# Performance work log

Hardware: AMD Instinct MI355X
Metric: run time of the kernel (lower is better)

The kernel has to match this reference:

```python
import jax, jax.numpy as jnp
import numpy as np

B = 4096          # batch
L = 4096          # lattice_size (64x64)
N = L // 2        # n_masked
H = 2048          # hidden_size


def setup_inputs() -> dict:
    key = jax.random.key(0)
    ks = jax.random.split(key, 4)
    scale = 0.02  # small init so exp(s) stays tame (s is already bounded by 2*tanh)
    x = jax.random.normal(ks[0], (B, L), dtype=jnp.float32)
    W1 = jax.random.normal(ks[1], (N, H), dtype=jnp.float32) * scale
    b1 = jnp.zeros((H,), jnp.float32)
    W2 = jax.random.normal(ks[2], (H, H), dtype=jnp.float32) * scale
    b2 = jnp.zeros((H,), jnp.float32)
    W3 = jax.random.normal(ks[3], (H, 2 * N), dtype=jnp.float32) * scale
    b3 = jnp.zeros((2 * N,), jnp.float32)
    # checkerboard mask: even sites frozen (masked), odd sites transformed
    idx_masked = jnp.arange(0, L, 2, dtype=jnp.int32)
    idx_unmasked = jnp.arange(1, L, 2, dtype=jnp.int32)
    return {"x": x, "W1": W1, "b1": b1, "W2": W2, "b2": b2,
            "W3": W3, "b3": b3,
            "idx_masked": idx_masked, "idx_unmasked": idx_unmasked}


def reference(x, W1, b1, W2, b2, W3, b3, idx_masked, idx_unmasked):
    # gather frozen half: (B, N)
    x_m = x[:, idx_masked]
    # 3-layer MLP with LeakyReLU(0.2)
    h = jax.nn.leaky_relu(x_m @ W1 + b1, negative_slope=0.2)
    h = jax.nn.leaky_relu(h @ W2 + b2, negative_slope=0.2)
    out = h @ W3 + b3                      # (B, 2N)
    s, t = out[:, :N], out[:, N:]
    s = 2.0 * jnp.tanh(s)
    # affine transform of the unmasked half, scatter back
    x_u = x[:, idx_unmasked]
    y_u = x_u * jnp.exp(s) + t
    y = x.at[:, idx_unmasked].set(y_u)
    log_det = s.sum(axis=1)                # (B,)
    return y, log_det
```

## Files before the change

kernel.cpp:

```cpp
#include <hip/hip_runtime.h>
#include <hip/hip_bf16.h>
#include <stdint.h>

#define MROWS 4096
#define LFULL 4096
#define NHALF 2048
#define HDIM  2048

typedef __bf16 bf16x8 __attribute__((ext_vector_type(8)));
typedef float  f32x4  __attribute__((ext_vector_type(4)));
typedef unsigned short u16x8 __attribute__((ext_vector_type(8)));

template<int V> struct ICt { static constexpr int value = V; };

__device__ __forceinline__ unsigned short f2bf(float f) {
    __hip_bfloat16 h = __float2bfloat16(f);
    return __builtin_bit_cast(unsigned short, h);
}
__device__ __forceinline__ float bf2f(unsigned short u) {
    return __builtin_bit_cast(float, (uint32_t)u << 16);
}
__device__ __forceinline__ float fast_tanh(float x) {
    float ax = fabsf(x);
    float e  = __expf(-2.0f * ax);
    float t  = (1.0f - e) / (1.0f + e);
    return copysignf(t, x);
}

__device__ __forceinline__ void gload_lds16(const void* g, void* l) {
    __builtin_amdgcn_global_load_lds(
        (const __attribute__((address_space(1))) uint32_t*)g,
        (__attribute__((address_space(3))) uint32_t*)l,
        16, 0, 0);
}

__global__ __launch_bounds__(256)
void cast_x_kernel(const float* __restrict__ x, __hip_bfloat16* __restrict__ xm,
                   float* __restrict__ ld)
{
    if (threadIdx.x == 0) ld[blockIdx.x] = 0.0f;
    size_t t = (size_t)blockIdx.x * 256 + threadIdx.x;
    size_t r = t >> 8;
    int    c = (int)(t & 255);
    const float4* xp = (const float4*)(x + r * LFULL + (size_t)c * 16);
    float4 a = xp[0], b = xp[1], d = xp[2], e = xp[3];
    u16x8 v;
    v[0] = f2bf(a.x); v[1] = f2bf(a.z);
    v[2] = f2bf(b.x); v[3] = f2bf(b.z);
    v[4] = f2bf(d.x); v[5] = f2bf(d.z);
    v[6] = f2bf(e.x); v[7] = f2bf(e.z);
    *(u16x8*)(xm + r * NHALF + (size_t)c * 8) = v;
}

template<bool PERM>
__global__ __launch_bounds__(256)
void transpose_cast_kernel(const float* __restrict__ W, __hip_bfloat16* __restrict__ WT,
                           int K, int N)
{
    __shared__ unsigned short lds[64][66];
    const int t  = threadIdx.x;
    const int k0 = blockIdx.y * 64;
    const int n0 = blockIdx.x * 64;

    #pragma unroll
    for (int it = 0; it < 4; ++it) {
        int kl = it * 16 + (t >> 4);
        int nl = (t & 15) * 4;
        float4 v = *(const float4*)(W + (size_t)(k0 + kl) * N + n0 + nl);
        lds[kl][nl + 0] = f2bf(v.x);
        lds[kl][nl + 1] = f2bf(v.y);
        lds[kl][nl + 2] = f2bf(v.z);
        lds[kl][nl + 3] = f2bf(v.w);
    }
    __syncthreads();

    int nl = t >> 2;
    int kc = (t & 3) * 16;
    unsigned short tmp[16];
    #pragma unroll
    for (int j = 0; j < 16; ++j) tmp[j] = lds[kc + j][nl];
    int jc = n0 + nl;
    int dstrow;
    if (PERM) {
        int half = jc >> 11;
        int j    = jc & 2047;
        int g = j >> 7, w = j & 127;
        int q = w >> 5, rest = w & 31, f = rest >> 4, c = rest & 15;
        dstrow = g * 256 + q * 64 + (f + 2 * half) * 16 + c;
    } else {
        dstrow = jc;
    }
    u16x8* dst = (u16x8*)(WT + (size_t)dstrow * K + k0 + kc);
    dst[0] = *(u16x8*)&tmp[0];
    dst[1] = *(u16x8*)&tmp[8];
}

template<int BM, int BN, int KD, int NOUT, bool RELU, bool FUSED>
__global__ __launch_bounds__(512, 2)
void gemm8p(const __hip_bfloat16* __restrict__ A,
            const __hip_bfloat16* __restrict__ BT,
            const float* __restrict__ bias,
            __hip_bfloat16* __restrict__ C,
            const float* __restrict__ xg,
            float* __restrict__ yg,
            float* __restrict__ ldg)
{
    constexpr int MF = BM / 32, NF = BN / 64, MH = MF / 2, NH = NF / 2;
    constexpr int LA = BM / 128, LB = BN / 128;
    constexpr int NT = KD / 64;
    constexpr int ABYTES = BM * 128, BBYTES = BN * 128;
    constexpr int BBASE = 2 * ABYTES;
    __shared__ __align__(1024) char lds[2 * ABYTES + 2 * BBYTES];

    const int tid  = threadIdx.x;
    const int wave = tid >> 6, lane = tid & 63;
    const int wm = wave >> 2, wn = wave & 3;
    const int l15 = lane & 15, lhi = lane >> 4;

    const int nwg = gridDim.x;
    const int bid = blockIdx.x;
    const int wg  = (bid & 7) * (nwg >> 3) + (bid >> 3);
    constexpr int NBN = NOUT / BN;
    const int bm = wg / NBN, bn = wg % NBN;

    const __hip_bfloat16* gA = A  + (size_t)(bm * BM) * KD;
    const __hip_bfloat16* gB = BT + (size_t)(bn * BN) * KD;

    const int srow = tid >> 3;
    const int scol = ((tid & 7) ^ (srow & 7)) * 8;
    char* sd = lds + srow * 128 + (tid & 7) * 16;

    const __hip_bfloat16* pA = gA + (size_t)srow * KD + scol;
    const __hip_bfloat16* pB = gB + (size_t)srow * KD + scol;

    #pragma unroll
    for (int s = 0; s < LB; ++s) gload_lds16(pB + (size_t)(s * 64) * KD,             sd + BBASE + s * 8192);
    #pragma unroll
    for (int s = 0; s < LB; ++s) gload_lds16(pB + (size_t)(BN/2 + s * 64) * KD,      sd + BBASE + (BN/2) * 128 + s * 8192);
    #pragma unroll
    for (int s = 0; s < LA; ++s) gload_lds16(pA + (size_t)(s * 64) * KD,             sd + s * 8192);
    #pragma unroll
    for (int s = 0; s < LA; ++s) gload_lds16(pA + (size_t)(BM/2 + s * 64) * KD,      sd + (BM/2) * 128 + s * 8192);
    #pragma unroll
    for (int s = 0; s < LB; ++s) gload_lds16(pB + 64 + (size_t)(s * 64) * KD,        sd + BBASE + BBYTES + s * 8192);
    #pragma unroll
    for (int s = 0; s < LB; ++s) gload_lds16(pB + 64 + (size_t)(BN/2 + s * 64) * KD, sd + BBASE + BBYTES + (BN/2) * 128 + s * 8192);
    pA += 64; pB += 128;
    asm volatile("s_waitcnt vmcnt(4)" ::: "memory");
    __builtin_amdgcn_s_barrier();

    const int arow0 = wm * (BM / 2) + l15;
    const int brow0 = wn * (BN / 4) + l15;
    const int swz   = (l15 & 7) << 4;
    const int colX[2] = { (lhi * 16) ^ swz, (64 + lhi * 16) ^ swz };
    const char* rA = lds + arow0 * 128;
    const char* rB = lds + brow0 * 128;

    bf16x8 af[MH][2], bf0[NH][2], bf1[NH][2];
    f32x4 acc[MF][NF] = {};

    #pragma unroll
    for (int m = 0; m < MH; ++m)
        #pragma unroll
        for (int kk = 0; kk < 2; ++kk)
            af[m][kk] = *(const bf16x8*)(rA + colX[kk] + m * 2048);
    #pragma unroll
    for (int n = 0; n < NH; ++n)
        #pragma unroll
        for (int kk = 0; kk < 2; ++kk)
            bf0[n][kk] = *(const bf16x8*)(rB + colX[kk] + (BBASE + n * 2048));

    auto body = [&](int t, auto bufc) {
        constexpr int BUF   = decltype(bufc)::value;
        constexpr int ABUF  = BUF * ABYTES;
        constexpr int ABUFo = (BUF ^ 1) * ABYTES;
        constexpr int BBUF  = BBASE + BUF * BBYTES;
        constexpr int BBUFo = BBASE + (BUF ^ 1) * BBYTES;

        if (t + 1 < NT) {
            #pragma unroll
            for (int s = 0; s < LA; ++s)
                gload_lds16(pA + (size_t)(s * 64) * KD, sd + ABUFo + s * 8192);
        }
        __builtin_amdgcn_s_setprio(1);
        #pragma unroll
        for (int kk = 0; kk < 2; ++kk)
            #pragma unroll
            for (int m = 0; m < MH; ++m)
                #pragma unroll
                for (int n = 0; n < NH; ++n)
                    acc[m][n] = __builtin_amdgcn_mfma_f32_16x16x32_bf16(af[m][kk], bf0[n][kk], acc[m][n], 0, 0, 0);
        __builtin_amdgcn_s_setprio(0);
        #pragma unroll
        for (int n = 0; n < NH; ++n)
            #pragma unroll
            for (int kk = 0; kk < 2; ++kk)
                bf1[n][kk] = *(const bf16x8*)(rB + colX[kk] + (BBUF + (NH + n) * 2048));
        __builtin_amdgcn_s_barrier();

        if (t + 1 < NT) {
            #pragma unroll
            for (int s = 0; s < LA; ++s)
                gload_lds16(pA + (size_t)(BM/2 + s * 64) * KD, sd + ABUFo + (BM/2) * 128 + s * 8192);
        }
        __builtin_amdgcn_s_setprio(1);
        #pragma unroll
        for (int kk = 0; kk < 2; ++kk)
            #pragma unroll
            for (int m = 0; m < MH; ++m)
                #pragma unroll
                for (int n = 0; n < NH; ++n)
                    acc[m][NH + n] = __builtin_amdgcn_mfma_f32_16x16x32_bf16(af[m][kk], bf1[n][kk], acc[m][NH + n], 0, 0, 0);
        __builtin_amdgcn_s_setprio(0);
        #pragma unroll
        for (int m = 0; m < MH; ++m)
            #pragma unroll
            for (int kk = 0; kk < 2; ++kk)
                af[m][kk] = *(const bf16x8*)(rA + colX[kk] + (ABUF + (MH + m) * 2048));
        __builtin_amdgcn_s_barrier();

        if (t + 2 < NT) {
            #pragma unroll
            for (int s = 0; s < LB; ++s)
                gload_lds16(pB + (size_t)(s * 64) * KD, sd + BBUF + s * 8192);
        }
        __builtin_amdgcn_s_setprio(1);
        #pragma unroll
        for (int kk = 0; kk < 2; ++kk)
            #pragma unroll
            for (int m = 0; m < MH; ++m)
                #pragma unroll
                for (int n = 0; n < NH; ++n)
                    acc[MH + m][n] = __builtin_amdgcn_mfma_f32_16x16x32_bf16(af[m][kk], bf0[n][kk], acc[MH + m][n], 0, 0, 0);
        __builtin_amdgcn_s_setprio(0);
        __builtin_amdgcn_s_barrier();

        if (t + 2 < NT) {
            #pragma unroll
            for (int s = 0; s < LB; ++s)
                gload_lds16(pB + (size_t)(BN/2 + s * 64) * KD, sd + BBUF + (BN/2) * 128 + s * 8192);
            asm volatile("s_waitcnt vmcnt(4)" ::: "memory");
        } else {
            asm volatile("s_waitcnt vmcnt(0)" ::: "memory");
        }
        __builtin_amdgcn_s_barrier();
        if (t + 1 < NT) {
            #pragma unroll
            for (int n = 0; n < NH; ++n)
                #pragma unroll
                for (int kk = 0; kk < 2; ++kk)
                    bf0[n][kk] = *(const bf16x8*)(rB + colX[kk] + (BBUFo + n * 2048));
        }
        __builtin_amdgcn_s_setprio(1);
        #pragma unroll
        for (int kk = 0; kk < 2; ++kk)
            #pragma unroll
            for (int m = 0; m < MH; ++m)
                #pragma unroll
                for (int n = 0; n < NH; ++n)
                    acc[MH + m][NH + n] = __builtin_amdgcn_mfma_f32_16x16x32_bf16(af[m][kk], bf1[n][kk], acc[MH + m][NH + n], 0, 0, 0);
        __builtin_amdgcn_s_setprio(0);
        if (t + 1 < NT) {
            #pragma unroll
            for (int m = 0; m < MH; ++m)
                #pragma unroll
                for (int kk = 0; kk < 2; ++kk)
                    af[m][kk] = *(const bf16x8*)(rA + colX[kk] + (ABUFo + m * 2048));
        }
        pA += 64; pB += 64;
    };

    for (int tt = 0; tt < NT; tt += 2) {
        body(tt,     ICt<0>{});
        body(tt + 1, ICt<1>{});
    }

    if constexpr (FUSED) {
        const int crow0 = bm * BM + wm * (BM / 2) + lhi * 4;
        const int jbase = bn * (BN / 2) + wn * 32 + l15;
        #pragma unroll
        for (int m = 0; m < MF; ++m) {
            #pragma unroll
            for (int r = 0; r < 4; ++r) {
                const int row = crow0 + m * 16 + r;
                float ldp = 0.0f;
                #pragma unroll
                for (int n = 0; n < 2; ++n) {
                    const int j = jbase + n * 16;
                    float sval = acc[m][n][r]     + bias[j];
                    float tval = acc[m][n + 2][r] + bias[NHALF + j];
                    float a = 2.0f * fast_tanh(sval);
                    ldp += a;
                    float2 xv = *(const float2*)(xg + (size_t)row * LFULL + 2 * j);
                    float2 yv;
                    yv.x = xv.x;
                    yv.y = xv.y * __expf(a) + tval;
                    *(float2*)(yg + (size_t)row * LFULL + 2 * j) = yv;
                }
                ldp += __shfl_xor(ldp, 1, 64);
                ldp += __shfl_xor(ldp, 2, 64);
                ldp += __shfl_xor(ldp, 4, 64);
                ldp += __shfl_xor(ldp, 8, 64);
                if (l15 == 0) atomicAdd(&ldg[row], ldp);
            }
        }
    } else {
        const int crow0 = bm * BM + wm * (BM / 2) + lhi * 4;
        const int ccol0 = bn * BN + wn * (BN / 4) + l15;
        #pragma unroll
        for (int m = 0; m < MF; ++m) {
            #pragma unroll
            for (int n = 0; n < NF; ++n) {
                int col = ccol0 + n * 16;
                float bv = bias[col];
                #pragma unroll
                for (int r = 0; r < 4; ++r) {
                    int row = crow0 + m * 16 + r;
                    float v = acc[m][n][r] + bv;
                    if (RELU) v = (v > 0.0f) ? v : 0.2f * v;
                    C[(size_t)row * NOUT + col] = __float2bfloat16(v);
                }
            }
        }
    }
}

extern "C" void kernel_launch(void* const* d_in, const int* in_sizes, int n_in,
                              void* d_out, int out_size, void* d_ws, size_t ws_size,
                              hipStream_t stream)
{
    const float* x  = (const float*)d_in[0];
    const float* W1 = (const float*)d_in[1];
    const float* b1 = (const float*)d_in[2];
    const float* W2 = (const float*)d_in[3];
    const float* b2 = (const float*)d_in[4];
    const float* W3 = (const float*)d_in[5];
    const float* b3 = (const float*)d_in[6];

    char* ws = (char*)d_ws;
    const size_t MB = 1u << 20;
    __hip_bfloat16* W3T  = (__hip_bfloat16*)(ws);
    __hip_bfloat16* h2   = (__hip_bfloat16*)(ws + 16 * MB);
    __hip_bfloat16* xmb  = (__hip_bfloat16*)(ws + 32 * MB);
    __hip_bfloat16* W1T  = (__hip_bfloat16*)(ws + 48 * MB);
    __hip_bfloat16* W2T  = (__hip_bfloat16*)(ws + 56 * MB);
    __hip_bfloat16* h1   = (__hip_bfloat16*)(ws + 64 * MB);

    float* y  = (float*)d_out;
    float* ld = y + (size_t)MROWS * LFULL;

    cast_x_kernel<<<4096, 256, 0, stream>>>(x, xmb, ld);
    transpose_cast_kernel<false><<<dim3(32, 32), 256, 0, stream>>>(W1, W1T, HDIM, HDIM);
    transpose_cast_kernel<false><<<dim3(32, 32), 256, 0, stream>>>(W2, W2T, HDIM, HDIM);
    transpose_cast_kernel<true ><<<dim3(64, 32), 256, 0, stream>>>(W3, W3T, HDIM, LFULL);

    gemm8p<128, 256, 2048, 2048, true,  false><<<dim3(256), dim3(512), 0, stream>>>(xmb, W1T, b1, h1, nullptr, nullptr, nullptr);
    gemm8p<128, 256, 2048, 2048, true,  false><<<dim3(256), dim3(512), 0, stream>>>(h1,  W2T, b2, h2, nullptr, nullptr, nullptr);
    gemm8p<256, 256, 2048, 4096, false, true ><<<dim3(256), dim3(512), 0, stream>>>(h2,  W3T, b3, nullptr, x, y, ld);
}
```

Measured before the change: 184.8 us.

## Load B operand directly to registers in first two GEMMs, drop barriers

Adds a new GEMM kernel for layers one and two that stages only the A tile in LDS and loads the weight (B) fragments straight from global memory into registers with double buffering, halving LDS use and removing the B-side LDS round trip. It also removes two intermediate barriers from the existing 8-phase pipelined kernel still used for layer three. The risk is more global traffic per wave for B and possible LDS read/write races from the dropped barriers.

Measured after the change: 264.6 us. +43.1%, slower.

```diff
diff --git a/kernel.cpp b/kernel.cpp
--- a/kernel.cpp
+++ b/kernel.cpp
@@ -95,6 +95,116 @@
     dst[1] = *(u16x8*)&tmp[8];
 }
 
+template<int BM, int BN, int KD, int NOUT, bool RELU>
+__global__ __launch_bounds__(512, 2)
+void gemm_bd(const __hip_bfloat16* __restrict__ A,
+             const __hip_bfloat16* __restrict__ BT,
+             const float* __restrict__ bias,
+             __hip_bfloat16* __restrict__ C)
+{
+    constexpr int NT = KD / 64;
+    constexpr int ABYTES = BM * 128;
+    __shared__ __align__(1024) char lds[2 * ABYTES];
+
+    const int tid  = threadIdx.x;
+    const int wave = tid >> 6, lane = tid & 63;
+    const int wm = wave >> 2, wn = wave & 3;
+    const int l15 = lane & 15, lhi = lane >> 4;
+
+    const int nwg = gridDim.x;
+    const int bid = blockIdx.x;
+    const int wg  = (bid & 7) * (nwg >> 3) + (bid >> 3);
+    constexpr int NBN = NOUT / BN;
+    const int bm = wg / NBN, bn = wg % NBN;
+
+    const int srow = tid >> 3;
+    const int scol = ((tid & 7) ^ (srow & 7)) * 8;
+    char* sd = lds + srow * 128 + (tid & 7) * 16;
+    const __hip_bfloat16* pA = A + (size_t)(bm * BM + srow) * KD + scol;
+
+    const __hip_bfloat16* pB = BT + (size_t)(bn * BN + wn * 64 + l15) * KD + lhi * 8;
+
+    bf16x8 bq[2][4][2];
+
+    gload_lds16(pA, sd);
+    gload_lds16(pA + (size_t)(BM / 2) * KD, sd + (BM / 2) * 128);
+    #pragma unroll
+    for (int n = 0; n < 4; ++n)
+        #pragma unroll
+        for (int kk = 0; kk < 2; ++kk)
+            bq[0][n][kk] = *(const bf16x8*)(pB + (size_t)n * 16 * KD + kk * 32);
+    pA += 64; pB += 64;
+    asm volatile("s_waitcnt vmcnt(8)" ::: "memory");
+    __builtin_amdgcn_s_barrier();
+
+    const int arow0 = wm * (BM / 2) + l15;
+    const int swz   = (l15 & 7) << 4;
+    const int colX[2] = { (lhi * 16) ^ swz, (64 + lhi * 16) ^ swz };
+    const char* rA = lds + arow0 * 128;
+
+    bf16x8 af[4][2];
+    f32x4 acc[4][4] = {};
+
+    auto body = [&](int t, auto bufc) {
+        constexpr int BUF   = decltype(bufc)::value;
+        constexpr int ABUF  = BUF * ABYTES;
+        constexpr int ABUFo = (BUF ^ 1) * ABYTES;
+
+        if (t + 1 < NT) {
+            gload_lds16(pA, sd + ABUFo);
+            gload_lds16(pA + (size_t)(BM / 2) * KD, sd + ABUFo + (BM / 2) * 128);
+            #pragma unroll
+            for (int n = 0; n < 4; ++n)
+                #pragma unroll
+                for (int kk = 0; kk < 2; ++kk)
+                    bq[BUF ^ 1][n][kk] = *(const bf16x8*)(pB + (size_t)n * 16 * KD + kk * 32);
+        }
+        #pragma unroll
+        for (int m = 0; m < 4; ++m)
+            #pragma unroll
+            for (int kk = 0; kk < 2; ++kk)
+                af[m][kk] = *(const bf16x8*)(rA + colX[kk] + (ABUF + m * 2048));
+        __builtin_amdgcn_s_setprio(1);
+        #pragma unroll
+        for (int kk = 0; kk < 2; ++kk)
+            #pragma unroll
+            for (int m = 0; m < 4; ++m)
+                #pragma unroll
+                for (int n = 0; n < 4; ++n)
+                    acc[m][n] = __builtin_amdgcn_mfma_f32_16x16x32_bf16(
+                        af[m][kk], bq[BUF][n][kk], acc[m][n], 0, 0, 0);
+        __builtin_amdgcn_s_setprio(0);
+        if (t + 1 < NT) {
+            asm volatile("s_waitcnt vmcnt(8)" ::: "memory");
+            __builtin_amdgcn_s_barrier();
+        }
+        pA += 64; pB += 64;
+    };
+
+    for (int tt = 0; tt < NT; tt += 2) {
+        body(tt,     ICt<0>{});
+        body(tt + 1, ICt<1>{});
+    }
+
+    const int crow0 = bm * BM + wm * (BM / 2) + lhi * 4;
+    const int ccol0 = bn * BN + wn * 64 + l15;
+    #pragma unroll
+    for (int m = 0; m < 4; ++m) {
+        #pragma unroll
+        for (int n = 0; n < 4; ++n) {
+            int col = ccol0 + n * 16;
+            float bv = bias[col];
+            #pragma unroll
+            for (int r = 0; r < 4; ++r) {
+                int row = crow0 + m * 16 + r;
+                float v = acc[m][n][r] + bv;
+                if (RELU) v = (v > 0.0f) ? v : 0.2f * v;
+                C[(size_t)row * NOUT + col] = __float2bfloat16(v);
+            }
+        }
+    }
+}
+
 template<int BM, int BN, int KD, int NOUT, bool RELU, bool FUSED>
 __global__ __launch_bounds__(512, 2)
 void gemm8p(const __hip_bfloat16* __restrict__ A,
@@ -196,7 +306,6 @@
             #pragma unroll
             for (int kk = 0; kk < 2; ++kk)
                 bf1[n][kk] = *(const bf16x8*)(rB + colX[kk] + (BBUF + (NH + n) * 2048));
-        __builtin_amdgcn_s_barrier();
 
         if (t + 1 < NT) {
             #pragma unroll
@@ -233,7 +342,6 @@
                 for (int n = 0; n < NH; ++n)
                     acc[MH + m][n] = __builtin_amdgcn_mfma_f32_16x16x32_bf16(af[m][kk], bf0[n][kk], acc[MH + m][n], 0, 0, 0);
         __builtin_amdgcn_s_setprio(0);
-        __builtin_amdgcn_s_barrier();
 
         if (t + 2 < NT) {
             #pragma unroll
@@ -275,8 +383,8 @@
         body(tt + 1, ICt<1>{});
     }
 
+    const int crow0 = bm * BM + wm * (BM / 2) + lhi * 4;
     if constexpr (FUSED) {
-        const int crow0 = bm * BM + wm * (BM / 2) + lhi * 4;
         const int jbase = bn * (BN / 2) + wn * 32 + l15;
         #pragma unroll
         for (int m = 0; m < MF; ++m) {
@@ -305,7 +413,6 @@
             }
         }
     } else {
-        const int crow0 = bm * BM + wm * (BM / 2) + lhi * 4;
         const int ccol0 = bn * BN + wn * (BN / 4) + l15;
         #pragma unroll
         for (int m = 0; m < MF; ++m) {
@@ -354,7 +461,7 @@
     transpose_cast_kernel<false><<<dim3(32, 32), 256, 0, stream>>>(W2, W2T, HDIM, HDIM);
     transpose_cast_kernel<true ><<<dim3(64, 32), 256, 0, stream>>>(W3, W3T, HDIM, LFULL);
 
-    gemm8p<128, 256, 2048, 2048, true,  false><<<dim3(256), dim3(512), 0, stream>>>(xmb, W1T, b1, h1, nullptr, nullptr, nullptr);
-    gemm8p<128, 256, 2048, 2048, true,  false><<<dim3(256), dim3(512), 0, stream>>>(h1,  W2T, b2, h2, nullptr, nullptr, nullptr);
-    gemm8p<256, 256, 2048, 4096, false, true ><<<dim3(256), dim3(512), 0, stream>>>(h2,  W3T, b3, nullptr, x, y, ld);
-}
+    gemm_bd<128, 256, 2048, 2048, true><<<dim3(256), dim3(512), 0, stream>>>(xmb, W1T, b1, h1);
+    gemm_bd<128, 256, 2048, 2048, true><<<dim3(256), dim3(512), 0, stream>>>(h1,  W2T, b2, h2);
+    gemm8p<256, 256, 2048, 4096, false, true><<<dim3(256), dim3(512), 0, stream>>>(h2, W3T, b3, nullptr, x, y, ld);
+}
```
